# Optimization experiments

Measured on AMD Instinct MI355X. Metric: run time of the kernel, lower is better.

The kernel has to match this reference:

```python
import jax, jax.numpy as jnp
import numpy as np

N_HEAD = 16
N_BLOCKS = 2
EPS = 1e-6

def _rmsnorm(x, g):
    return x * jax.lax.rsqrt(jnp.mean(x * x, axis=-1, keepdims=True) + EPS) * g

def _causal_sa(x, Wqkv, Wproj, g):
    # x: (B, T, C); fused qkv, RMSNorm on q/k over full C before head split
    B, T, C = x.shape
    hd = C // N_HEAD
    q, k, v = jnp.split(x @ Wqkv, 3, axis=-1)
    q = _rmsnorm(q, g)
    k = _rmsnorm(k, g)
    def heads(t):
        return t.reshape(B, T, N_HEAD, hd).transpose(0, 2, 1, 3)
    q, k, v = heads(q), heads(k), heads(v)
    scores = jnp.einsum('bhqd,bhkd->bhqk', q, k) * (1.0 / np.sqrt(hd))
    mask = jnp.tril(jnp.ones((T, T), dtype=bool))
    scores = jnp.where(mask, scores, -jnp.finfo(scores.dtype).max)
    att = jax.nn.softmax(scores, axis=-1)
    y = jnp.einsum('bhqk,bhkd->bhqd', att, v)
    y = y.transpose(0, 2, 1, 3).reshape(B, T, C)
    return y @ Wproj

def setup_inputs() -> dict:
    key = jax.random.key(0)
    ks = jax.random.split(key, 8)
    B, ng, T, C = 2, 8, 256, 1024
    M_loc, M_glob = 16, 16
    s = 0.02
    return {
        'x': jax.random.normal(ks[0], (B, ng, T, C), jnp.float32),
        'mem_tokens': jax.random.normal(ks[1], (B, M_glob, C), jnp.float32),
        'local_mem': jax.random.normal(ks[2], (B, ng, M_loc, C), jnp.float32),
        'Wqkv_loc': jax.random.normal(ks[3], (N_BLOCKS, C, 3 * C), jnp.float32) * s,
        'Wproj_loc': jax.random.normal(ks[4], (N_BLOCKS, C, C), jnp.float32) * s,
        'g_loc': jnp.ones((N_BLOCKS, C), jnp.float32),
        'Wqkv_glob': jax.random.normal(ks[5], (N_BLOCKS, C, 3 * C), jnp.float32) * s,
        'Wproj_glob': jax.random.normal(ks[6], (N_BLOCKS, C, C), jnp.float32) * s,
        'g_glob': jnp.ones((N_BLOCKS, C), jnp.float32),
    }

def reference(x, mem_tokens, local_mem, Wqkv_loc, Wproj_loc, g_loc, Wqkv_glob, Wproj_glob, g_glob):
    B, ng, T, C = x.shape
    M_loc = local_mem.shape[2]
    M_glob = mem_tokens.shape[1]
    for i in range(N_BLOCKS):
        # local causal SA: per-group, with local mem tokens prepended
        xl = jnp.concatenate([local_mem, x], axis=2).reshape(B * ng, M_loc + T, C)
        yl = _causal_sa(xl, Wqkv_loc[i], Wproj_loc[i], g_loc[i])
        yl = yl.reshape(B, ng, M_loc + T, C)
        local_mem = yl[:, :, :M_loc, :]
        x = yl[:, :, M_loc:, :]
        # global causal SA over flattened sequence with global mem tokens
        xg = x.reshape(B, ng * T, C)
        xg = jnp.concatenate([mem_tokens, xg], axis=1)
        yg = _causal_sa(xg, Wqkv_glob[i], Wproj_glob[i], g_glob[i])
        mem_tokens = yg[:, :M_glob, :]
        x = yg[:, M_glob:, :].reshape(B, ng, T, C)
    return x
```

## Files before the change

### kernel.cpp

```cpp
#include <hip/hip_runtime.h>
#include <hip/hip_bf16.h>
#include <math.h>

typedef __attribute__((ext_vector_type(8))) short s16x8;
typedef __attribute__((ext_vector_type(4))) short s16x4;
typedef __attribute__((ext_vector_type(4))) float f32x4;

#define MPAD 4352

__device__ __forceinline__ short f2b(float f) {
  unsigned u = __float_as_uint(f);
  unsigned r = (u + 0x7fffu + ((u >> 16) & 1u)) >> 16;
  return (short)(unsigned short)r;
}
__device__ __forceinline__ float b2f(short s) {
  return __uint_as_float(((unsigned)(unsigned short)s) << 16);
}

__device__ __forceinline__ void gl_lds16(const short* g, short* l) {
  __builtin_amdgcn_global_load_lds((const __attribute__((address_space(1))) short*)g,
                                   (__attribute__((address_space(3))) short*)l, 16, 0, 0);
}

__global__ __launch_bounds__(256) void transpose_cast(const float* __restrict__ in,
                                                      short* __restrict__ out,
                                                      int K, int N) {
  __shared__ float tile[32][33];
  int bn = blockIdx.x * 32;
  int bk = blockIdx.y * 32;
  for (int i = threadIdx.y; i < 32; i += 8)
    tile[i][threadIdx.x] = in[(size_t)(bk + i) * N + bn + threadIdx.x];
  __syncthreads();
  for (int i = threadIdx.y; i < 32; i += 8)
    out[(size_t)(bn + i) * K + bk + threadIdx.x] = f2b(tile[threadIdx.x][i]);
}

__global__ __launch_bounds__(256) void transpose_v(const short* __restrict__ QKV,
                                                   short* __restrict__ Vt,
                                                   int L, int Lpad) {
  __shared__ short tile[32][33];
  int sh = blockIdx.z;
  int s = sh >> 4, h = sh & 15;
  int kb = blockIdx.x * 32;
  int cb = blockIdx.y * 32;
  int tx = threadIdx.x;
  for (int i = threadIdx.y; i < 32; i += 8) {
    int key = kb + i;
    if (key > L - 1) key = L - 1;
    tile[i][tx] = QKV[(size_t)(s * L + key) * 3072 + 2048 + h * 64 + cb + tx];
  }
  __syncthreads();
  for (int i = threadIdx.y; i < 32; i += 8)
    Vt[((size_t)sh * 64 + cb + i) * Lpad + kb + tx] = tile[tx][i];
}

__global__ __launch_bounds__(256) void gemm_bt2(const short* __restrict__ A,
                                                const short* __restrict__ BT,
                                                short* __restrict__ C,
                                                int K, int N) {
  __shared__ short As[128 * 32];
  __shared__ short Bs[128 * 32];
  const int tid = threadIdx.x;
  const int lane = tid & 63;
  const int w = tid >> 6;
  const int wr = (w >> 1) * 64, wc = (w & 1) * 64;
  const int m0 = blockIdx.y * 128;
  const int n0 = blockIdx.x * 128;
  const int l15 = lane & 15, lhi = lane >> 4;

  f32x4 acc[4][4] = {};

  for (int k0 = 0; k0 < K; k0 += 32) {
    __syncthreads();
#pragma unroll
    for (int p = 0; p < 2; ++p) {
      int g = w * 128 + p * 64 + lane;
      int row = g >> 2;
      int cs = (g & 3) * 8;
      gl_lds16(A + (size_t)(m0 + row) * K + k0 + cs, &As[g * 8]);
      gl_lds16(BT + (size_t)(n0 + row) * K + k0 + cs, &Bs[g * 8]);
    }
    __syncthreads();
    s16x8 af[4], bf[4];
#pragma unroll
    for (int m = 0; m < 4; ++m)
      af[m] = *(const s16x8*)(&As[(wr + m * 16 + l15) * 32 + lhi * 8]);
#pragma unroll
    for (int n = 0; n < 4; ++n)
      bf[n] = *(const s16x8*)(&Bs[(wc + n * 16 + l15) * 32 + lhi * 8]);
#pragma unroll
    for (int m = 0; m < 4; ++m)
#pragma unroll
      for (int n = 0; n < 4; ++n)
        acc[m][n] = __builtin_amdgcn_mfma_f32_16x16x32_bf16(af[m], bf[n], acc[m][n], 0, 0, 0);
  }
#pragma unroll
  for (int m = 0; m < 4; ++m) {
    int row_base = m0 + wr + m * 16 + lhi * 4;
#pragma unroll
    for (int n = 0; n < 4; ++n) {
      int col = n0 + wc + n * 16 + l15;
#pragma unroll
      for (int r = 0; r < 4; ++r)
        C[(size_t)(row_base + r) * N + col] = f2b(acc[m][n][r]);
    }
  }
}

__global__ __launch_bounds__(256) void rmsnorm_qk(short* __restrict__ QKV,
                                                  const float* __restrict__ g) {
  int row = blockIdx.x;
  int which = blockIdx.y;
  size_t base = (size_t)row * 3072 + (size_t)which * 1024;
  int t = threadIdx.x;
  s16x4 in = *(const s16x4*)(QKV + base + t * 4);
  float v[4];
  float ss = 0.f;
#pragma unroll
  for (int j = 0; j < 4; ++j) {
    v[j] = b2f(in[j]);
    ss += v[j] * v[j];
  }
#pragma unroll
  for (int m = 32; m >= 1; m >>= 1) ss += __shfl_xor(ss, m);
  __shared__ float red[4];
  if ((t & 63) == 0) red[t >> 6] = ss;
  __syncthreads();
  float tot = red[0] + red[1] + red[2] + red[3];
  float inv = rsqrtf(tot * (1.0f / 1024.0f) + 1e-6f);
  if (which == 0) inv *= 0.125f;
  s16x4 out;
#pragma unroll
  for (int j = 0; j < 4; ++j) out[j] = f2b(v[j] * inv * g[t * 4 + j]);
  *(s16x4*)(&QKV[base + t * 4]) = out;
}

__global__ __launch_bounds__(256) void attn_causal3(const short* __restrict__ QKV,
                                                    const short* __restrict__ Vt,
                                                    short* __restrict__ Y,
                                                    int L, int Lpad) {
  const int h = blockIdx.y, s = blockIdx.z;
  const int q0 = blockIdx.x * 64;
  const int tid = threadIdx.x;
  const int lane = tid & 63, w = tid >> 6;
  const int l15 = lane & 15, lhi = lane >> 4;
  const int row0 = s * L;

  __shared__ short Ks[64][72];
  __shared__ short Vs[2][64][72];
  __shared__ short Ps[4][16][72];

  int qld = q0 + w * 16 + l15;
  if (qld > L - 1) qld = L - 1;
  const size_t qrow = (size_t)(row0 + qld) * 3072 + h * 64;
  s16x8 qf0 = *(const s16x8*)(QKV + qrow + lhi * 8);
  s16x8 qf1 = *(const s16x8*)(QKV + qrow + 32 + lhi * 8);

  float lsum[4] = {0.f, 0.f, 0.f, 0.f};
  f32x4 o[4];
#pragma unroll
  for (int d = 0; d < 4; ++d) o[d] = f32x4{0.f, 0.f, 0.f, 0.f};

  const short* Vbase = Vt + (size_t)(s * 16 + h) * 64 * Lpad;

  s16x8 kreg[2], vreg[2];
#pragma unroll
  for (int p = 0; p < 2; ++p) {
    int g = tid + p * 256;
    int kr = g >> 3, cs = (g & 7) * 8;
    int krow = kr;
    if (krow > L - 1) krow = L - 1;
    kreg[p] = *(const s16x8*)(QKV + (size_t)(row0 + krow) * 3072 + 1024 + h * 64 + cs);
    vreg[p] = *(const s16x8*)(Vbase + (size_t)kr * Lpad + cs);
  }

  int buf = 0;
  for (int kb = 0; kb <= q0; kb += 64, buf ^= 1) {
#pragma unroll
    for (int p = 0; p < 2; ++p) {
      int g = tid + p * 256;
      int kr = g >> 3, cs = (g & 7) * 8;
      *(s16x8*)(&Ks[kr][cs]) = kreg[p];
      *(s16x8*)(&Vs[buf][kr][cs]) = vreg[p];
    }
    if (kb + 64 <= q0) {
#pragma unroll
      for (int p = 0; p < 2; ++p) {
        int g = tid + p * 256;
        int kr = g >> 3, cs = (g & 7) * 8;
        int krow = kb + 64 + kr;
        if (krow > L - 1) krow = L - 1;
        kreg[p] = *(const s16x8*)(QKV + (size_t)(row0 + krow) * 3072 + 1024 + h * 64 + cs);
        vreg[p] = *(const s16x8*)(Vbase + (size_t)kr * Lpad + kb + 64 + cs);
      }
    }
    __syncthreads();

    f32x4 st[4];
#pragma unroll
    for (int n = 0; n < 4; ++n) {
      s16x8 k0 = *(const s16x8*)(&Ks[n * 16 + l15][lhi * 8]);
      s16x8 k1 = *(const s16x8*)(&Ks[n * 16 + l15][32 + lhi * 8]);
      f32x4 sa = f32x4{0.f, 0.f, 0.f, 0.f};
      sa = __builtin_amdgcn_mfma_f32_16x16x32_bf16(qf0, k0, sa, 0, 0, 0);
      sa = __builtin_amdgcn_mfma_f32_16x16x32_bf16(qf1, k1, sa, 0, 0, 0);
      st[n] = sa;
    }

    if (kb == q0) {
#pragma unroll
      for (int n = 0; n < 4; ++n) {
        int key = kb + n * 16 + l15;
#pragma unroll
        for (int r = 0; r < 4; ++r) {
          int qr = q0 + w * 16 + lhi * 4 + r;
          if (key > qr) st[n][r] = -1e30f;
        }
      }
    }

#pragma unroll
    for (int n = 0; n < 4; ++n) {
#pragma unroll
      for (int r = 0; r < 4; ++r) {
        float p = __expf(st[n][r] - 8.0f);
        Ps[w][lhi * 4 + r][n * 16 + l15] = f2b(p);
        lsum[r] += p;
      }
    }
    __syncthreads();

#pragma unroll
    for (int kk = 0; kk < 2; ++kk) {
      s16x8 pa = *(const s16x8*)(&Ps[w][l15][kk * 32 + lhi * 8]);
#pragma unroll
      for (int d = 0; d < 4; ++d) {
        s16x8 vf = *(const s16x8*)(&Vs[buf][d * 16 + l15][kk * 32 + lhi * 8]);
        o[d] = __builtin_amdgcn_mfma_f32_16x16x32_bf16(pa, vf, o[d], 0, 0, 0);
      }
    }
  }

#pragma unroll
  for (int r = 0; r < 4; ++r) {
#pragma unroll
    for (int mm = 1; mm <= 8; mm <<= 1) lsum[r] += __shfl_xor(lsum[r], mm, 16);
  }
#pragma unroll
  for (int d = 0; d < 4; ++d) {
#pragma unroll
    for (int r = 0; r < 4; ++r) {
      int qr = q0 + w * 16 + lhi * 4 + r;
      if (qr < L)
        Y[(size_t)(row0 + qr) * 1024 + h * 64 + d * 16 + l15] = f2b(o[d][r] / lsum[r]);
    }
  }
}

__global__ __launch_bounds__(256) void build_xl(const float* __restrict__ x,
                                                const float* __restrict__ lm,
                                                short* __restrict__ Xin) {
  int row = blockIdx.x;
  int s = row / 272, r = row % 272;
  const float* src = (r < 16) ? lm + ((size_t)s * 16 + r) * 1024
                              : x + ((size_t)s * 256 + (r - 16)) * 1024;
  int t = threadIdx.x;
  f32x4 v = *(const f32x4*)(src + t * 4);
  s16x4 o;
#pragma unroll
  for (int j = 0; j < 4; ++j) o[j] = f2b(v[j]);
  *(s16x4*)(&Xin[(size_t)row * 1024 + t * 4]) = o;
}

__global__ __launch_bounds__(256) void build_xg(const float* __restrict__ x,
                                                const float* __restrict__ mem,
                                                short* __restrict__ Xin) {
  int row = blockIdx.x;
  int sr = row < 4128 ? row : 4127;
  int b = sr / 2064, r = sr % 2064;
  const float* src = (r < 16) ? mem + ((size_t)b * 16 + r) * 1024
                              : x + ((size_t)b * 2048 + (r - 16)) * 1024;
  int t = threadIdx.x;
  f32x4 v = *(const f32x4*)(src + t * 4);
  s16x4 o;
#pragma unroll
  for (int j = 0; j < 4; ++j) o[j] = f2b(v[j]);
  *(s16x4*)(&Xin[(size_t)row * 1024 + t * 4]) = o;
}

__global__ __launch_bounds__(256) void split_local(const short* __restrict__ Pout,
                                                   float* __restrict__ x,
                                                   float* __restrict__ lm) {
  int row = blockIdx.x;
  int s = row / 272, r = row % 272;
  int t = threadIdx.x;
  s16x4 v = *(const s16x4*)(Pout + (size_t)row * 1024 + t * 4);
  float* dst = (r < 16) ? lm + ((size_t)s * 16 + r) * 1024
                        : x + ((size_t)s * 256 + (r - 16)) * 1024;
  f32x4 o;
#pragma unroll
  for (int j = 0; j < 4; ++j) o[j] = b2f(v[j]);
  *(f32x4*)(dst + t * 4) = o;
}

__global__ __launch_bounds__(256) void split_global(const short* __restrict__ Pout,
                                                    float* __restrict__ x,
                                                    float* __restrict__ mem) {
  int row = blockIdx.x;
  int b = row / 2064, r = row % 2064;
  int t = threadIdx.x;
  s16x4 v = *(const s16x4*)(Pout + (size_t)row * 1024 + t * 4);
  float* dst = (r < 16) ? mem + ((size_t)b * 16 + r) * 1024
                        : x + ((size_t)b * 2048 + (r - 16)) * 1024;
  f32x4 o;
#pragma unroll
  for (int j = 0; j < 4; ++j) o[j] = b2f(v[j]);
  *(f32x4*)(dst + t * 4) = o;
}

extern "C" void kernel_launch(void* const* d_in, const int* in_sizes, int n_in,
                              void* d_out, int out_size, void* d_ws, size_t ws_size,
                              hipStream_t stream) {
  const float* x_in = (const float*)d_in[0];
  const float* mem_in = (const float*)d_in[1];
  const float* lm_in = (const float*)d_in[2];
  const float* Wqkv_loc = (const float*)d_in[3];
  const float* Wproj_loc = (const float*)d_in[4];
  const float* g_loc = (const float*)d_in[5];
  const float* Wqkv_glob = (const float*)d_in[6];
  const float* Wproj_glob = (const float*)d_in[7];
  const float* g_glob = (const float*)d_in[8];

  char* ws = (char*)d_ws;
  size_t off = 0;
  auto alloc = [&](size_t bytes) {
    char* p = ws + off;
    off += (bytes + 255) & ~(size_t)255;
    return p;
  };
  short* Wt = (short*)alloc((size_t)3072 * 1024 * 2);
  float* x_cur = (float*)alloc((size_t)4096 * 1024 * 4);
  float* lm_cur = (float*)alloc((size_t)256 * 1024 * 4);
  float* mem_cur = (float*)alloc((size_t)32 * 1024 * 4);
  short* Xin = (short*)alloc((size_t)MPAD * 1024 * 2);
  short* QKVb = (short*)alloc((size_t)MPAD * 3072 * 2);
  short* Yb = (short*)alloc((size_t)MPAD * 1024 * 2);
  short* Pout = (short*)alloc((size_t)MPAD * 1024 * 2);
  short* Vtb = (short*)alloc((size_t)256 * 64 * 320 * 2);

  hipMemcpyAsync(x_cur, x_in, (size_t)4096 * 1024 * 4, hipMemcpyDeviceToDevice, stream);
  hipMemcpyAsync(lm_cur, lm_in, (size_t)256 * 1024 * 4, hipMemcpyDeviceToDevice, stream);
  hipMemcpyAsync(mem_cur, mem_in, (size_t)32 * 1024 * 4, hipMemcpyDeviceToDevice, stream);

  for (int i = 0; i < 2; ++i) {
    transpose_cast<<<dim3(96, 32), dim3(32, 8), 0, stream>>>(
        Wqkv_loc + (size_t)i * 1024 * 3072, Wt, 1024, 3072);
    build_xl<<<4352, 256, 0, stream>>>(x_cur, lm_cur, Xin);
    gemm_bt2<<<dim3(24, 34), 256, 0, stream>>>(Xin, Wt, QKVb, 1024, 3072);
    rmsnorm_qk<<<dim3(4352, 2), 256, 0, stream>>>(QKVb, g_loc + (size_t)i * 1024);
    transpose_v<<<dim3(10, 2, 256), dim3(32, 8), 0, stream>>>(QKVb, Vtb, 272, 320);
    attn_causal3<<<dim3(5, 16, 16), 256, 0, stream>>>(QKVb, Vtb, Yb, 272, 320);
    transpose_cast<<<dim3(32, 32), dim3(32, 8), 0, stream>>>(
        Wproj_loc + (size_t)i * 1024 * 1024, Wt, 1024, 1024);
    gemm_bt2<<<dim3(8, 34), 256, 0, stream>>>(Yb, Wt, Pout, 1024, 1024);
    split_local<<<4352, 256, 0, stream>>>(Pout, x_cur, lm_cur);

    transpose_cast<<<dim3(96, 32), dim3(32, 8), 0, stream>>>(
        Wqkv_glob + (size_t)i * 1024 * 3072, Wt, 1024, 3072);
    build_xg<<<4352, 256, 0, stream>>>(x_cur, mem_cur, Xin);
    gemm_bt2<<<dim3(24, 34), 256, 0, stream>>>(Xin, Wt, QKVb, 1024, 3072);
    rmsnorm_qk<<<dim3(4128, 2), 256, 0, stream>>>(QKVb, g_glob + (size_t)i * 1024);
    transpose_v<<<dim3(66, 2, 32), dim3(32, 8), 0, stream>>>(QKVb, Vtb, 2064, 2112);
    attn_causal3<<<dim3(33, 16, 2), 256, 0, stream>>>(QKVb, Vtb, Yb, 2064, 2112);
    transpose_cast<<<dim3(32, 32), dim3(32, 8), 0, stream>>>(
        Wproj_glob + (size_t)i * 1024 * 1024, Wt, 1024, 1024);
    gemm_bt2<<<dim3(8, 34), 256, 0, stream>>>(Yb, Wt, Pout, 1024, 1024);
    split_global<<<4128, 256, 0, stream>>>(Pout, x_cur, mem_cur);
  }

  hipMemcpyAsync(d_out, x_cur, (size_t)4096 * 1024 * 4, hipMemcpyDeviceToDevice, stream);
}
```

Baseline: 638.6 us.

## Split global causal attention over key chunks with atomic accumulation and merge

Global causal attention is now split along the key dimension into chunks of 8 key tiles, one block per (query tile, chunk, head). Each block atomically adds its unnormalized partial output and row sums into fp32 buffers, and a separate merge kernel divides and writes bf16. The goal is to fix the load imbalance and low parallelism of the causal per-query-tile kernel on the long global sequence. The cost is two memsets, fp32 atomics, an extra kernel launch and extra workspace, and it depends on the fixed-offset exponent that has no running max.

```diff
diff --git a/kernel.cpp b/kernel.cpp
--- a/kernel.cpp
+++ b/kernel.cpp
@@ -7,6 +7,8 @@
 typedef __attribute__((ext_vector_type(4))) float f32x4;
 
 #define MPAD 4352
+#define LG 2064
+#define CT 8
 
 __device__ __forceinline__ short f2b(float f) {
   unsigned u = __float_as_uint(f);
@@ -254,6 +256,152 @@
       if (qr < L)
         Y[(size_t)(row0 + qr) * 1024 + h * 64 + d * 16 + l15] = f2b(o[d][r] / lsum[r]);
     }
+  }
+}
+
+__global__ __launch_bounds__(256) void attn_split(const short* __restrict__ QKV,
+                                                  const short* __restrict__ Vt,
+                                                  float* __restrict__ o_acc,
+                                                  float* __restrict__ ls_acc) {
+  const int qb = blockIdx.x;
+  const int chunk = blockIdx.y;
+  const int sh = blockIdx.z;
+  const int t0 = chunk * CT;
+  if (t0 > qb) return;
+  const int t1 = min(t0 + CT, qb + 1);
+  const int h = sh & 15, s = sh >> 4;
+  const int q0 = qb * 64;
+  const int tid = threadIdx.x;
+  const int lane = tid & 63, w = tid >> 6;
+  const int l15 = lane & 15, lhi = lane >> 4;
+  const int row0 = s * LG;
+  const int Lpad = 2112;
+
+  __shared__ short Ks[64][72];
+  __shared__ short Vs[2][64][72];
+  __shared__ short Ps[4][16][72];
+
+  int qld = q0 + w * 16 + l15;
+  if (qld > LG - 1) qld = LG - 1;
+  const size_t qrow = (size_t)(row0 + qld) * 3072 + h * 64;
+  s16x8 qf0 = *(const s16x8*)(QKV + qrow + lhi * 8);
+  s16x8 qf1 = *(const s16x8*)(QKV + qrow + 32 + lhi * 8);
+
+  float lsum[4] = {0.f, 0.f, 0.f, 0.f};
+  f32x4 o[4];
+#pragma unroll
+  for (int d = 0; d < 4; ++d) o[d] = f32x4{0.f, 0.f, 0.f, 0.f};
+
+  const short* Vbase = Vt + (size_t)sh * 64 * Lpad;
+
+  s16x8 kreg[2], vreg[2];
+  const int kb0 = t0 * 64;
+#pragma unroll
+  for (int p = 0; p < 2; ++p) {
+    int g = tid + p * 256;
+    int kr = g >> 3, cs = (g & 7) * 8;
+    int krow = kb0 + kr;
+    if (krow > LG - 1) krow = LG - 1;
+    kreg[p] = *(const s16x8*)(QKV + (size_t)(row0 + krow) * 3072 + 1024 + h * 64 + cs);
+    vreg[p] = *(const s16x8*)(Vbase + (size_t)kr * Lpad + kb0 + cs);
+  }
+
+  int buf = 0;
+  for (int t = t0; t < t1; ++t, buf ^= 1) {
+    const int kb = t * 64;
+#pragma unroll
+    for (int p = 0; p < 2; ++p) {
+      int g = tid + p * 256;
+      int kr = g >> 3, cs = (g & 7) * 8;
+      *(s16x8*)(&Ks[kr][cs]) = kreg[p];
+      *(s16x8*)(&Vs[buf][kr][cs]) = vreg[p];
+    }
+    if (t + 1 < t1) {
+#pragma unroll
+      for (int p = 0; p < 2; ++p) {
+        int g = tid + p * 256;
+        int kr = g >> 3, cs = (g & 7) * 8;
+        int krow = kb + 64 + kr;
+        if (krow > LG - 1) krow = LG - 1;
+        kreg[p] = *(const s16x8*)(QKV + (size_t)(row0 + krow) * 3072 + 1024 + h * 64 + cs);
+        vreg[p] = *(const s16x8*)(Vbase + (size_t)kr * Lpad + kb + 64 + cs);
+      }
+    }
+    __syncthreads();
+
+    f32x4 st[4];
+#pragma unroll
+    for (int n = 0; n < 4; ++n) {
+      s16x8 k0 = *(const s16x8*)(&Ks[n * 16 + l15][lhi * 8]);
+      s16x8 k1 = *(const s16x8*)(&Ks[n * 16 + l15][32 + lhi * 8]);
+      f32x4 sa = f32x4{0.f, 0.f, 0.f, 0.f};
+      sa = __builtin_amdgcn_mfma_f32_16x16x32_bf16(qf0, k0, sa, 0, 0, 0);
+      sa = __builtin_amdgcn_mfma_f32_16x16x32_bf16(qf1, k1, sa, 0, 0, 0);
+      st[n] = sa;
+    }
+
+    if (t == qb) {
+#pragma unroll
+      for (int n = 0; n < 4; ++n) {
+        int key = kb + n * 16 + l15;
+#pragma unroll
+        for (int r = 0; r < 4; ++r) {
+          int qr = q0 + w * 16 + lhi * 4 + r;
+          if (key > qr) st[n][r] = -1e30f;
+        }
+      }
+    }
+
+#pragma unroll
+    for (int n = 0; n < 4; ++n) {
+#pragma unroll
+      for (int r = 0; r < 4; ++r) {
+        float p = __expf(st[n][r] - 8.0f);
+        Ps[w][lhi * 4 + r][n * 16 + l15] = f2b(p);
+        lsum[r] += p;
+      }
+    }
+    __syncthreads();
+
+#pragma unroll
+    for (int kk = 0; kk < 2; ++kk) {
+      s16x8 pa = *(const s16x8*)(&Ps[w][l15][kk * 32 + lhi * 8]);
+#pragma unroll
+      for (int d = 0; d < 4; ++d) {
+        s16x8 vf = *(const s16x8*)(&Vs[buf][d * 16 + l15][kk * 32 + lhi * 8]);
+        o[d] = __builtin_amdgcn_mfma_f32_16x16x32_bf16(pa, vf, o[d], 0, 0, 0);
+      }
+    }
+  }
+
+#pragma unroll
+  for (int r = 0; r < 4; ++r) {
+#pragma unroll
+    for (int mm = 1; mm <= 8; mm <<= 1) lsum[r] += __shfl_xor(lsum[r], mm, 16);
+  }
+#pragma unroll
+  for (int r = 0; r < 4; ++r) {
+    int qr = q0 + w * 16 + lhi * 4 + r;
+    if (qr < LG) {
+      if (l15 == 0) atomicAdd(&ls_acc[(size_t)sh * LG + qr], lsum[r]);
+#pragma unroll
+      for (int d = 0; d < 4; ++d)
+        atomicAdd(&o_acc[((size_t)sh * LG + qr) * 64 + d * 16 + l15], o[d][r]);
+    }
+  }
+}
+
+__global__ __launch_bounds__(256) void attn_merge(const float* __restrict__ o_acc,
+                                                  const float* __restrict__ ls_acc,
+                                                  short* __restrict__ Y) {
+  int sh = blockIdx.z * 16 + blockIdx.y;
+  int s = sh >> 4, h = sh & 15;
+  int row = blockIdx.x * 4 + (threadIdx.x >> 6);
+  int col = threadIdx.x & 63;
+  if (row < LG) {
+    float inv = 1.0f / ls_acc[(size_t)sh * LG + row];
+    float v = o_acc[((size_t)sh * LG + row) * 64 + col];
+    Y[(size_t)(s * LG + row) * 1024 + h * 64 + col] = f2b(v * inv);
   }
 }
 
@@ -347,6 +495,11 @@
   short* Yb = (short*)alloc((size_t)MPAD * 1024 * 2);
   short* Pout = (short*)alloc((size_t)MPAD * 1024 * 2);
   short* Vtb = (short*)alloc((size_t)256 * 64 * 320 * 2);
+  size_t oacc_bytes = (size_t)32 * LG * 64 * 4;
+  size_t lacc_bytes = (size_t)32 * LG * 4;
+  float* o_acc = (float*)alloc(oacc_bytes);
+  float* ls_acc = (float*)alloc(lacc_bytes);
+  const bool use_split = (ws_size >= off);
 
   hipMemcpyAsync(x_cur, x_in, (size_t)4096 * 1024 * 4, hipMemcpyDeviceToDevice, stream);
   hipMemcpyAsync(lm_cur, lm_in, (size_t)256 * 1024 * 4, hipMemcpyDeviceToDevice, stream);
@@ -371,7 +524,14 @@
     gemm_bt2<<<dim3(24, 34), 256, 0, stream>>>(Xin, Wt, QKVb, 1024, 3072);
     rmsnorm_qk<<<dim3(4128, 2), 256, 0, stream>>>(QKVb, g_glob + (size_t)i * 1024);
     transpose_v<<<dim3(66, 2, 32), dim3(32, 8), 0, stream>>>(QKVb, Vtb, 2064, 2112);
-    attn_causal3<<<dim3(33, 16, 2), 256, 0, stream>>>(QKVb, Vtb, Yb, 2064, 2112);
+    if (use_split) {
+      hipMemsetAsync(o_acc, 0, oacc_bytes, stream);
+      hipMemsetAsync(ls_acc, 0, lacc_bytes, stream);
+      attn_split<<<dim3(33, 5, 32), 256, 0, stream>>>(QKVb, Vtb, o_acc, ls_acc);
+      attn_merge<<<dim3(516, 16, 2), 256, 0, stream>>>(o_acc, ls_acc, Yb);
+    } else {
+      attn_causal3<<<dim3(33, 16, 2), 256, 0, stream>>>(QKVb, Vtb, Yb, 2064, 2112);
+    }
     transpose_cast<<<dim3(32, 32), dim3(32, 8), 0, stream>>>(
         Wproj_glob + (size_t)i * 1024 * 1024, Wt, 1024, 1024);
     gemm_bt2<<<dim3(8, 34), 256, 0, stream>>>(Yb, Wt, Pout, 1024, 1024);
```

Measured after the change: 655.8 us. 1.03x slower.
